# Kernel tuning notes

Measured on AMD Instinct MI355X. Metric: run time of the kernel, lower is better.

The kernel has to match this reference:

```python
import jax, jax.numpy as jnp
import numpy as np

EPS = 1e-5  # torch LayerNorm default eps

def _ln(x, g, b):
    mu = jnp.mean(x, axis=-1, keepdims=True)
    var = jnp.mean((x - mu) ** 2, axis=-1, keepdims=True)
    return (x - mu) * jax.lax.rsqrt(var + EPS) * g + b

def setup_inputs() -> dict:
    key = jax.random.key(0)
    ks = jax.random.split(key, 8)
    B, N, F, E, H = 8, 512, 64, 16, 4
    node = jax.random.normal(ks[0], (B, N, F), jnp.float32)
    edge = jax.random.normal(ks[1], (B, N, N, E), jnp.float32)
    adj = jax.random.randint(ks[2], (B, N, N), 0, 2, jnp.int32)
    s = lambda k, shp, fan: jax.random.normal(k, shp, jnp.float32) / np.sqrt(fan).astype(np.float32)
    return dict(
        node=node, edge=edge, adj=adj,
        ln1_g=jnp.ones((F,), jnp.float32), ln1_b=jnp.zeros((F,), jnp.float32),
        Wn=s(ks[3], (F, F), F), bn=jnp.zeros((F,), jnp.float32),
        ln2_g=jnp.ones((E,), jnp.float32), ln2_b=jnp.zeros((E,), jnp.float32),
        We1=s(ks[4], (2 * E, E), E), be1=jnp.zeros((2 * E,), jnp.float32),
        We2=s(ks[5], (E, 2 * E), 2 * E), be2=jnp.zeros((E,), jnp.float32),
        lne_g=jnp.ones((E,), jnp.float32), lne_b=jnp.zeros((E,), jnp.float32),
        attn_A=s(ks[6], (H, 2 * (F // H) + E), F // H),
        Wo=s(ks[7], (F, F), F), bo=jnp.zeros((F,), jnp.float32),
        lno_g=jnp.ones((F,), jnp.float32), lno_b=jnp.zeros((F,), jnp.float32),
    )

def reference(node, edge, adj, ln1_g, ln1_b, Wn, bn, ln2_g, ln2_b, We1, be1, We2, be2, lne_g, lne_b, attn_A, Wo, bo, lno_g, lno_b):
    B, N, F = node.shape
    H = attn_A.shape[0]
    hd = F // H
    node_res = node
    # node projection (dropout = identity at eval)
    h = _ln(node, ln1_g, ln1_b) @ Wn.T + bn                         # (B,N,F)
    # edge MLP with residual + layer norm
    e = _ln(edge, ln2_g, ln2_b)
    e = jax.nn.celu(e @ We1.T + be1) @ We2.T + be2
    e = _ln(e + edge, lne_g, lne_b)                                  # (B,N,N,E)
    h = h.reshape(B, N, H, hd)
    # (concat @ attn_matrix.T).sum(-1) == concat . attn_matrix.sum(0)
    a = attn_A.sum(0)                                                # (2*hd+E,)
    a_row, a_col, a_edge = a[:hd], a[hd:2 * hd], a[2 * hd:]
    sr = jnp.einsum('bnhx,x->bnh', h, a_row)                         # row term (b,i,h)
    sc = jnp.einsum('bnhx,x->bnh', h, a_col)                         # col term (b,j,h)
    se = jnp.einsum('bije,e->bij', e, a_edge)                        # edge term (b,i,j)
    logits = sr[:, :, None, :] + sc[:, None, :, :] + se[..., None]   # (B,N,N,H)
    logits = jnp.where(adj[..., None] == 0, jnp.float32(-1e9), logits)
    logits = jax.nn.leaky_relu(logits, 0.2)
    logits = jnp.clip(logits, -1e9, 1e9)
    coeffs = jax.nn.softmax(logits, axis=2)                          # softmax over j
    coeffs = jnp.nan_to_num(coeffs, nan=0.0)
    # msg[b,n,h,x] = sum_m h[b,m,h,x] * coeffs[b,n,m,h]
    msg = jnp.einsum('bmhx,bnmh->bnhx', h, coeffs).reshape(B, N, F)
    out = msg @ Wo.T + bo + node_res                                 # residual_proj == Identity (in==out)
    out = jax.nn.leaky_relu(out, 0.2)
    out = _ln(out, lno_g, lno_b)
    return (out, e, adj)
```

## Files before the change

kernel.cpp:

```cpp
#include <hip/hip_runtime.h>

#define EPS 1e-5f

__device__ __forceinline__ float wave_sum64(float v) {
    #pragma unroll
    for (int off = 32; off > 0; off >>= 1) v += __shfl_xor(v, off, 64);
    return v;
}
__device__ __forceinline__ float wave_max64(float v) {
    #pragma unroll
    for (int off = 32; off > 0; off >>= 1) v = fmaxf(v, __shfl_xor(v, off, 64));
    return v;
}

__global__ __launch_bounds__(64) void node_kernel(
    const float* __restrict__ node, const float* __restrict__ ln1_g, const float* __restrict__ ln1_b,
    const float* __restrict__ Wn, const float* __restrict__ bn, const float* __restrict__ attn_A,
    float* __restrict__ h_out, float* __restrict__ sr_out, float* __restrict__ sc_out)
{
    const int row  = blockIdx.x;
    const int lane = threadIdx.x;

    float x = node[(long)row * 64 + lane];
    float mu  = wave_sum64(x) * (1.0f / 64.0f);
    float d   = x - mu;
    float var = wave_sum64(d * d) * (1.0f / 64.0f);
    float xln = d * rsqrtf(var + EPS) * ln1_g[lane] + ln1_b[lane];

    __shared__ float xs[64];
    xs[lane] = xln;
    __syncthreads();

    float acc = bn[lane];
    const float* wrow = Wn + lane * 64;
    #pragma unroll
    for (int f = 0; f < 64; ++f) acc = fmaf(xs[f], wrow[f], acc);
    h_out[(long)row * 64 + lane] = acc;

    const int xidx = lane & 15;
    float ar = 0.f, ac = 0.f;
    #pragma unroll
    for (int hh = 0; hh < 4; ++hh) {
        ar += attn_A[hh * 48 + xidx];
        ac += attn_A[hh * 48 + 16 + xidx];
    }
    float pr = acc * ar, pc = acc * ac;
    #pragma unroll
    for (int off = 8; off > 0; off >>= 1) {
        pr += __shfl_down(pr, off, 16);
        pc += __shfl_down(pc, off, 16);
    }
    if (xidx == 0) {
        const int head = lane >> 4;
        sr_out[(long)row * 4 + head] = pr;
        sc_out[(long)row * 4 + head] = pc;
    }
}

__global__ __launch_bounds__(256) void edge_kernel(
    const float* __restrict__ edge, const int* __restrict__ adj,
    const float* __restrict__ ln2_g, const float* __restrict__ ln2_b,
    const float* __restrict__ We1, const float* __restrict__ be1,
    const float* __restrict__ We2, const float* __restrict__ be2,
    const float* __restrict__ lne_g, const float* __restrict__ lne_b,
    const float* __restrict__ attn_A,
    float* __restrict__ e_out, float* __restrict__ adj_out, float* __restrict__ se_out)
{
    const long r = (long)blockIdx.x * 256 + threadIdx.x;

    const float4* ep = (const float4*)(edge + r * 16);
    float4 v0 = ep[0], v1 = ep[1], v2 = ep[2], v3 = ep[3];
    float ev[16] = { v0.x, v0.y, v0.z, v0.w, v1.x, v1.y, v1.z, v1.w,
                     v2.x, v2.y, v2.z, v2.w, v3.x, v3.y, v3.z, v3.w };

    float mu = 0.f;
    #pragma unroll
    for (int i = 0; i < 16; ++i) mu += ev[i];
    mu *= (1.0f / 16.0f);
    float var = 0.f;
    #pragma unroll
    for (int i = 0; i < 16; ++i) { float d = ev[i] - mu; var += d * d; }
    var *= (1.0f / 16.0f);
    const float rs = rsqrtf(var + EPS);

    float xln[16];
    #pragma unroll
    for (int i = 0; i < 16; ++i) xln[i] = (ev[i] - mu) * rs * ln2_g[i] + ln2_b[i];

    float act[32];
    #pragma unroll
    for (int k = 0; k < 32; ++k) {
        float a = be1[k];
        #pragma unroll
        for (int i = 0; i < 16; ++i) a = fmaf(xln[i], We1[k * 16 + i], a);
        act[k] = (a > 0.f) ? a : (__expf(a) - 1.f);
    }

    float eo[16];
    #pragma unroll
    for (int j = 0; j < 16; ++j) {
        float a = be2[j];
        #pragma unroll
        for (int k = 0; k < 32; ++k) a = fmaf(act[k], We2[j * 32 + k], a);
        eo[j] = a + ev[j];
    }

    float mu2 = 0.f;
    #pragma unroll
    for (int j = 0; j < 16; ++j) mu2 += eo[j];
    mu2 *= (1.0f / 16.0f);
    float var2 = 0.f;
    #pragma unroll
    for (int j = 0; j < 16; ++j) { float d = eo[j] - mu2; var2 += d * d; }
    var2 *= (1.0f / 16.0f);
    const float rs2 = rsqrtf(var2 + EPS);

    float se = 0.f;
    #pragma unroll
    for (int j = 0; j < 16; ++j) {
        float ae = attn_A[32 + j] + attn_A[48 + 32 + j] + attn_A[96 + 32 + j] + attn_A[144 + 32 + j];
        float o = (eo[j] - mu2) * rs2 * lne_g[j] + lne_b[j];
        eo[j] = o;
        se = fmaf(o, ae, se);
    }

    float4* op = (float4*)(e_out + r * 16);
    op[0] = make_float4(eo[0], eo[1], eo[2], eo[3]);
    op[1] = make_float4(eo[4], eo[5], eo[6], eo[7]);
    op[2] = make_float4(eo[8], eo[9], eo[10], eo[11]);
    op[3] = make_float4(eo[12], eo[13], eo[14], eo[15]);

    se_out[r]  = se;
    adj_out[r] = (float)adj[r];
}

__global__ __launch_bounds__(256) void attn_kernel(
    const float* __restrict__ h_ws, const float* __restrict__ sr_ws, const float* __restrict__ sc_ws,
    const float* __restrict__ se_ws, const int* __restrict__ adj,
    const float* __restrict__ node, const float* __restrict__ Wo, const float* __restrict__ bo,
    const float* __restrict__ lno_g, const float* __restrict__ lno_b,
    float* __restrict__ out)
{
    const int bi   = blockIdx.x;
    const int b    = bi >> 9;
    const int tid  = threadIdx.x;
    const int wave = tid >> 6;
    const int lane = tid & 63;

    __shared__ float lg[4][520];
    __shared__ float msg_p[4][64];
    __shared__ float msg_l[64];

    const float sr0 = sr_ws[(long)bi * 4 + 0];
    const float sr1 = sr_ws[(long)bi * 4 + 1];
    const float sr2 = sr_ws[(long)bi * 4 + 2];
    const float sr3 = sr_ws[(long)bi * 4 + 3];

    const float*  se_row  = se_ws + (long)bi * 512;
    const int*    adj_row = adj   + (long)bi * 512;
    const float4* sc4     = (const float4*)(sc_ws + (long)b * 512 * 4);

    for (int j = tid; j < 512; j += 256) {
        float4 s = sc4[j];
        float  se = se_row[j];
        bool   m  = (adj_row[j] != 0);
        float l0 = m ? (sr0 + s.x + se) : -1e9f;
        float l1 = m ? (sr1 + s.y + se) : -1e9f;
        float l2 = m ? (sr2 + s.z + se) : -1e9f;
        float l3 = m ? (sr3 + s.w + se) : -1e9f;
        l0 = (l0 > 0.f) ? l0 : 0.2f * l0;  l0 = fminf(fmaxf(l0, -1e9f), 1e9f);
        l1 = (l1 > 0.f) ? l1 : 0.2f * l1;  l1 = fminf(fmaxf(l1, -1e9f), 1e9f);
        l2 = (l2 > 0.f) ? l2 : 0.2f * l2;  l2 = fminf(fmaxf(l2, -1e9f), 1e9f);
        l3 = (l3 > 0.f) ? l3 : 0.2f * l3;  l3 = fminf(fmaxf(l3, -1e9f), 1e9f);
        lg[0][j] = l0; lg[1][j] = l1; lg[2][j] = l2; lg[3][j] = l3;
    }
    __syncthreads();

    {
        float* L = lg[wave];
        float v[8];
        float m = -1e30f;
        #pragma unroll
        for (int k = 0; k < 8; ++k) { v[k] = L[lane + k * 64]; m = fmaxf(m, v[k]); }
        m = wave_max64(m);
        float s = 0.f;
        #pragma unroll
        for (int k = 0; k < 8; ++k) { v[k] = __expf(v[k] - m); s += v[k]; }
        s = wave_sum64(s);
        const float inv = 1.0f / s;
        #pragma unroll
        for (int k = 0; k < 8; ++k) L[lane + k * 64] = v[k] * inv;
    }
    __syncthreads();

    {
        const int f    = lane;
        const int head = f >> 4;
        const float* hb = h_ws + (long)b * 512 * 64;
        float acc = 0.f;
        const int j0 = wave * 128;
        #pragma unroll 4
        for (int j = j0; j < j0 + 128; ++j)
            acc = fmaf(hb[(long)j * 64 + f], lg[head][j], acc);
        msg_p[wave][lane] = acc;
    }
    __syncthreads();

    if (tid < 64) {
        msg_l[lane] = msg_p[0][lane] + msg_p[1][lane] + msg_p[2][lane] + msg_p[3][lane];
    }
    __syncthreads();

    if (tid < 64) {
        float o = bo[lane];
        const float* wrow = Wo + lane * 64;
        #pragma unroll
        for (int ff = 0; ff < 64; ++ff) o = fmaf(msg_l[ff], wrow[ff], o);
        o += node[(long)bi * 64 + lane];
        o = (o > 0.f) ? o : 0.2f * o;
        float mu  = wave_sum64(o) * (1.0f / 64.0f);
        float d   = o - mu;
        float var = wave_sum64(d * d) * (1.0f / 64.0f);
        out[(long)bi * 64 + lane] = d * rsqrtf(var + EPS) * lno_g[lane] + lno_b[lane];
    }
}

extern "C" void kernel_launch(void* const* d_in, const int* in_sizes, int n_in,
                              void* d_out, int out_size, void* d_ws, size_t ws_size,
                              hipStream_t stream) {
    const float* node   = (const float*)d_in[0];
    const float* edge   = (const float*)d_in[1];
    const int*   adj    = (const int*)  d_in[2];
    const float* ln1_g  = (const float*)d_in[3];
    const float* ln1_b  = (const float*)d_in[4];
    const float* Wn     = (const float*)d_in[5];
    const float* bn     = (const float*)d_in[6];
    const float* ln2_g  = (const float*)d_in[7];
    const float* ln2_b  = (const float*)d_in[8];
    const float* We1    = (const float*)d_in[9];
    const float* be1    = (const float*)d_in[10];
    const float* We2    = (const float*)d_in[11];
    const float* be2    = (const float*)d_in[12];
    const float* lne_g  = (const float*)d_in[13];
    const float* lne_b  = (const float*)d_in[14];
    const float* attn_A = (const float*)d_in[15];
    const float* Wo     = (const float*)d_in[16];
    const float* bo     = (const float*)d_in[17];
    const float* lno_g  = (const float*)d_in[18];
    const float* lno_b  = (const float*)d_in[19];

    float* out_p  = (float*)d_out;
    float* e_out  = out_p + 262144;
    float* adj_o  = e_out + 33554432;

    float* ws    = (float*)d_ws;
    float* h_ws  = ws;
    float* sr_ws = ws + 262144;
    float* sc_ws = ws + 278528;
    float* se_ws = ws + 294912;

    node_kernel<<<4096, 64, 0, stream>>>(node, ln1_g, ln1_b, Wn, bn, attn_A, h_ws, sr_ws, sc_ws);
    edge_kernel<<<8192, 256, 0, stream>>>(edge, adj, ln2_g, ln2_b, We1, be1, We2, be2,
                                          lne_g, lne_b, attn_A, e_out, adj_o, se_ws);
    attn_kernel<<<4096, 256, 0, stream>>>(h_ws, sr_ws, sc_ws, se_ws, adj, node,
                                          Wo, bo, lno_g, lno_b, out_p);
}
```

Measured before the change: 355.2 us.

## Process four query rows per attention block to reuse h loads

The attention kernel now handles four consecutive rows per block, so each load of the h matrix feeds four accumulators instead of one. The grid shrinks fourfold, and all four waves now do the output projection and layer norm instead of only one. The edge kernel hoists the attention-vector sums ahead of the main work, and both kernels gain a min-blocks-per-CU launch bound. The coefficient buffer grows to about 33KB of shared memory per block, which can limit occupancy.

```diff
diff --git a/kernel.cpp b/kernel.cpp
--- a/kernel.cpp
+++ b/kernel.cpp
@@ -57,7 +57,7 @@
     }
 }
 
-__global__ __launch_bounds__(256) void edge_kernel(
+__global__ __launch_bounds__(256, 4) void edge_kernel(
     const float* __restrict__ edge, const int* __restrict__ adj,
     const float* __restrict__ ln2_g, const float* __restrict__ ln2_b,
     const float* __restrict__ We1, const float* __restrict__ be1,
@@ -73,6 +73,11 @@
     float ev[16] = { v0.x, v0.y, v0.z, v0.w, v1.x, v1.y, v1.z, v1.w,
                      v2.x, v2.y, v2.z, v2.w, v3.x, v3.y, v3.z, v3.w };
 
+    float ae[16];
+    #pragma unroll
+    for (int j = 0; j < 16; ++j)
+        ae[j] = attn_A[32 + j] + attn_A[48 + 32 + j] + attn_A[96 + 32 + j] + attn_A[144 + 32 + j];
+
     float mu = 0.f;
     #pragma unroll
     for (int i = 0; i < 16; ++i) mu += ev[i];
@@ -118,10 +123,9 @@
     float se = 0.f;
     #pragma unroll
     for (int j = 0; j < 16; ++j) {
-        float ae = attn_A[32 + j] + attn_A[48 + 32 + j] + attn_A[96 + 32 + j] + attn_A[144 + 32 + j];
         float o = (eo[j] - mu2) * rs2 * lne_g[j] + lne_b[j];
         eo[j] = o;
-        se = fmaf(o, ae, se);
+        se = fmaf(o, ae[j], se);
     }
 
     float4* op = (float4*)(e_out + r * 16);
@@ -134,50 +138,58 @@
     adj_out[r] = (float)adj[r];
 }
 
-__global__ __launch_bounds__(256) void attn_kernel(
+#define G 4
+__global__ __launch_bounds__(256, 4) void attn_kernel(
     const float* __restrict__ h_ws, const float* __restrict__ sr_ws, const float* __restrict__ sc_ws,
     const float* __restrict__ se_ws, const int* __restrict__ adj,
     const float* __restrict__ node, const float* __restrict__ Wo, const float* __restrict__ bo,
     const float* __restrict__ lno_g, const float* __restrict__ lno_b,
     float* __restrict__ out)
 {
-    const int bi   = blockIdx.x;
-    const int b    = bi >> 9;
+    const int bi0  = blockIdx.x * G;
+    const int b    = bi0 >> 9;
     const int tid  = threadIdx.x;
     const int wave = tid >> 6;
     const int lane = tid & 63;
 
-    __shared__ float lg[4][520];
-    __shared__ float msg_p[4][64];
-    __shared__ float msg_l[64];
-
-    const float sr0 = sr_ws[(long)bi * 4 + 0];
-    const float sr1 = sr_ws[(long)bi * 4 + 1];
-    const float sr2 = sr_ws[(long)bi * 4 + 2];
-    const float sr3 = sr_ws[(long)bi * 4 + 3];
-
-    const float*  se_row  = se_ws + (long)bi * 512;
-    const int*    adj_row = adj   + (long)bi * 512;
-    const float4* sc4     = (const float4*)(sc_ws + (long)b * 512 * 4);
-
-    for (int j = tid; j < 512; j += 256) {
-        float4 s = sc4[j];
-        float  se = se_row[j];
-        bool   m  = (adj_row[j] != 0);
-        float l0 = m ? (sr0 + s.x + se) : -1e9f;
-        float l1 = m ? (sr1 + s.y + se) : -1e9f;
-        float l2 = m ? (sr2 + s.z + se) : -1e9f;
-        float l3 = m ? (sr3 + s.w + se) : -1e9f;
-        l0 = (l0 > 0.f) ? l0 : 0.2f * l0;  l0 = fminf(fmaxf(l0, -1e9f), 1e9f);
-        l1 = (l1 > 0.f) ? l1 : 0.2f * l1;  l1 = fminf(fmaxf(l1, -1e9f), 1e9f);
-        l2 = (l2 > 0.f) ? l2 : 0.2f * l2;  l2 = fminf(fmaxf(l2, -1e9f), 1e9f);
-        l3 = (l3 > 0.f) ? l3 : 0.2f * l3;  l3 = fminf(fmaxf(l3, -1e9f), 1e9f);
-        lg[0][j] = l0; lg[1][j] = l1; lg[2][j] = l2; lg[3][j] = l3;
-    }
-    __syncthreads();
-
-    {
-        float* L = lg[wave];
+    __shared__ float coef[G][4][516];
+    __shared__ float hpart[4][G][64];
+    __shared__ float msg_s[G][64];
+
+    const float4* sc4 = (const float4*)(sc_ws + (long)b * 512 * 4);
+
+    #pragma unroll
+    for (int r = 0; r < G; ++r) {
+        const int row = bi0 + r;
+        const float sr0 = sr_ws[(long)row * 4 + 0];
+        const float sr1 = sr_ws[(long)row * 4 + 1];
+        const float sr2 = sr_ws[(long)row * 4 + 2];
+        const float sr3 = sr_ws[(long)row * 4 + 3];
+        const float* se_row  = se_ws + (long)row * 512;
+        const int*   adj_row = adj   + (long)row * 512;
+        #pragma unroll
+        for (int half = 0; half < 2; ++half) {
+            const int j = half * 256 + tid;
+            float4 s = sc4[j];
+            float  se = se_row[j];
+            bool   m  = (adj_row[j] != 0);
+            float l0 = m ? (sr0 + s.x + se) : -1e9f;
+            float l1 = m ? (sr1 + s.y + se) : -1e9f;
+            float l2 = m ? (sr2 + s.z + se) : -1e9f;
+            float l3 = m ? (sr3 + s.w + se) : -1e9f;
+            l0 = (l0 > 0.f) ? l0 : 0.2f * l0;  l0 = fminf(fmaxf(l0, -1e9f), 1e9f);
+            l1 = (l1 > 0.f) ? l1 : 0.2f * l1;  l1 = fminf(fmaxf(l1, -1e9f), 1e9f);
+            l2 = (l2 > 0.f) ? l2 : 0.2f * l2;  l2 = fminf(fmaxf(l2, -1e9f), 1e9f);
+            l3 = (l3 > 0.f) ? l3 : 0.2f * l3;  l3 = fminf(fmaxf(l3, -1e9f), 1e9f);
+            coef[r][0][j] = l0; coef[r][1][j] = l1; coef[r][2][j] = l2; coef[r][3][j] = l3;
+        }
+    }
+    __syncthreads();
+
+    #pragma unroll
+    for (int q = 0; q < 4; ++q) {
+        const int p = q * 4 + wave;
+        float* L = coef[p >> 2][p & 3];
         float v[8];
         float m = -1e30f;
         #pragma unroll
@@ -194,34 +206,41 @@
     __syncthreads();
 
     {
-        const int f    = lane;
-        const int head = f >> 4;
+        const int head = lane >> 4;
         const float* hb = h_ws + (long)b * 512 * 64;
-        float acc = 0.f;
+        float a0 = 0.f, a1 = 0.f, a2 = 0.f, a3 = 0.f;
         const int j0 = wave * 128;
-        #pragma unroll 4
-        for (int j = j0; j < j0 + 128; ++j)
-            acc = fmaf(hb[(long)j * 64 + f], lg[head][j], acc);
-        msg_p[wave][lane] = acc;
-    }
-    __syncthreads();
-
-    if (tid < 64) {
-        msg_l[lane] = msg_p[0][lane] + msg_p[1][lane] + msg_p[2][lane] + msg_p[3][lane];
-    }
-    __syncthreads();
-
-    if (tid < 64) {
+        #pragma unroll 8
+        for (int j = j0; j < j0 + 128; ++j) {
+            float hv = hb[(long)j * 64 + lane];
+            a0 = fmaf(hv, coef[0][head][j], a0);
+            a1 = fmaf(hv, coef[1][head][j], a1);
+            a2 = fmaf(hv, coef[2][head][j], a2);
+            a3 = fmaf(hv, coef[3][head][j], a3);
+        }
+        hpart[wave][0][lane] = a0;
+        hpart[wave][1][lane] = a1;
+        hpart[wave][2][lane] = a2;
+        hpart[wave][3][lane] = a3;
+    }
+    __syncthreads();
+
+    {
+        const int r   = wave;
+        const int row = bi0 + r;
+        float m = hpart[0][r][lane] + hpart[1][r][lane] + hpart[2][r][lane] + hpart[3][r][lane];
+        msg_s[r][lane] = m;
+
         float o = bo[lane];
         const float* wrow = Wo + lane * 64;
         #pragma unroll
-        for (int ff = 0; ff < 64; ++ff) o = fmaf(msg_l[ff], wrow[ff], o);
-        o += node[(long)bi * 64 + lane];
+        for (int ff = 0; ff < 64; ++ff) o = fmaf(msg_s[r][ff], wrow[ff], o);
+        o += node[(long)row * 64 + lane];
         o = (o > 0.f) ? o : 0.2f * o;
         float mu  = wave_sum64(o) * (1.0f / 64.0f);
         float d   = o - mu;
         float var = wave_sum64(d * d) * (1.0f / 64.0f);
-        out[(long)bi * 64 + lane] = d * rsqrtf(var + EPS) * lno_g[lane] + lno_b[lane];
+        out[(long)row * 64 + lane] = d * rsqrtf(var + EPS) * lno_g[lane] + lno_b[lane];
     }
 }
 
@@ -262,6 +281,6 @@
     node_kernel<<<4096, 64, 0, stream>>>(node, ln1_g, ln1_b, Wn, bn, attn_A, h_ws, sr_ws, sc_ws);
     edge_kernel<<<8192, 256, 0, stream>>>(edge, adj, ln2_g, ln2_b, We1, be1, We2, be2,
                                           lne_g, lne_b, attn_A, e_out, adj_o, se_ws);
-    attn_kernel<<<4096, 256, 0, stream>>>(h_ws, sr_ws, sc_ws, se_ws, adj, node,
+    attn_kernel<<<1024, 256, 0, stream>>>(h_ws, sr_ws, sc_ws, se_ws, adj, node,
                                           Wo, bo, lno_g, lno_b, out_p);
 }
```

New measurement: 344.7 us. -3.0%, faster.
